# Kernel optimization log

Measured on AMD Instinct MI355X. Metric: run time of the kernel, lower is better.

Reference implementation:

```python
import jax, jax.numpy as jnp
import numpy as np

D_SIZE = 64
BATCH = 4096

def setup_inputs() -> dict:
    key = jax.random.key(0)
    n_vec = D_SIZE * (D_SIZE - 1) // 2  # 2016
    S_vec = jax.random.normal(key, (BATCH, n_vec), dtype=jnp.float32)
    return {"S_vec": S_vec}

def reference(S_vec):
    d = D_SIZE
    iu, ju = np.triu_indices(d, k=1)  # row-major strict upper triangle, same as torch.triu_indices(d, d, 1)
    # Scatter into skew-symmetric matrix: upper = -S_vec, lower = +S_vec
    S = jnp.zeros((*S_vec.shape[:-1], d, d), dtype=S_vec.dtype)
    S = S.at[..., iu, ju].set(-S_vec)
    S = S.at[..., ju, iu].set(S_vec)
    # 1j*S is Hermitian -> real eigenvalues w; original D = w/1j = -1j*w
    w, V = jnp.linalg.eigh(1j * S.astype(jnp.complex64))
    exp_D = jnp.exp(-1j * w)  # exp(D) with D purely imaginary
    # (V * exp_D) @ V^H, take real part (exp of skew-sym is real orthogonal)
    out = (V * exp_D[..., None, :]) @ jnp.conj(jnp.swapaxes(V, -1, -2))
    return out.real
```

## Files before the change

kernel.cpp:

```cpp
#include <hip/hip_runtime.h>
#include <math.h>

#define NVEC 2016
#define NT   256
#define KMAX 8

typedef __attribute__((ext_vector_type(8))) short short8;
typedef __attribute__((ext_vector_type(4))) float v4f;

#define MFMA(a,b,c) __builtin_amdgcn_mfma_f32_16x16x32_bf16((a),(b),(c),0,0,0)

static __device__ __forceinline__ unsigned cvtpk(float a, float b){
    unsigned r;
    asm("v_cvt_pk_bf16_f32 %0, %1, %2" : "=v"(r) : "v"(a), "v"(b));
    return r;
}

static __device__ __forceinline__ void pack_hl4(const float x[4], uint2 &H, uint2 &L){
    H.x = cvtpk(x[0], x[1]);
    H.y = cvtpk(x[2], x[3]);
    float r0 = x[0] - __uint_as_float(H.x << 16);
    float r1 = x[1] - __uint_as_float(H.x & 0xFFFF0000u);
    float r2 = x[2] - __uint_as_float(H.y << 16);
    float r3 = x[3] - __uint_as_float(H.y & 0xFFFF0000u);
    L.x = cvtpk(r0, r1);
    L.y = cvtpk(r2, r3);
}

static __device__ __forceinline__ int swz(int maj, int g){ return maj*64 + ((g ^ (maj & 7)) << 3); }
static __device__ __forceinline__ int swe(int maj, int t){ return swz(maj, t >> 3) + (t & 7); }

static __device__ __forceinline__ short8 ldp(const unsigned short* P, int maj, int off){
    return *(const short8*)&P[swz(maj, off >> 3)];
}

static __device__ __forceinline__ short8 neg8(short8 a){
    union { unsigned u[4]; short8 s; } X; X.s = a;
    X.u[0]^=0x80008000u; X.u[1]^=0x80008000u; X.u[2]^=0x80008000u; X.u[3]^=0x80008000u;
    return X.s;
}

static __device__ __forceinline__ void pair4(const unsigned short* Ph, const unsigned short* Pl,
                                             int cc, int row0, float o[4]){
    const int base = swe(cc, row0);
    uint2 h = *(const uint2*)&Ph[base];
    uint2 l = *(const uint2*)&Pl[base];
    o[0] = __uint_as_float(h.x<<16)           + __uint_as_float(l.x<<16);
    o[1] = __uint_as_float(h.x & 0xFFFF0000u) + __uint_as_float(l.x & 0xFFFF0000u);
    o[2] = __uint_as_float(h.y<<16)           + __uint_as_float(l.y<<16);
    o[3] = __uint_as_float(h.y & 0xFFFF0000u) + __uint_as_float(l.y & 0xFFFF0000u);
}

static __device__ __forceinline__ void pair4h(const unsigned short* Ph, int cc, int row0, float o[4]){
    const uint2 h = *(const uint2*)&Ph[swe(cc, row0)];
    o[0] = __uint_as_float(h.x<<16);
    o[1] = __uint_as_float(h.x & 0xFFFF0000u);
    o[2] = __uint_as_float(h.y<<16);
    o[3] = __uint_as_float(h.y & 0xFFFF0000u);
}

__global__ void __launch_bounds__(NT, 4)
SkewSymMatrixExp_kernel(const float* __restrict__ vin, float* __restrict__ out)
{
    __shared__ __attribute__((aligned(16))) unsigned short PAh[4096];
    __shared__ __attribute__((aligned(16))) unsigned short PAl[4096];
    __shared__ __attribute__((aligned(16))) unsigned short P2h[4096];
    __shared__ __attribute__((aligned(16))) unsigned short P2l[4096];
    __shared__ __attribute__((aligned(16))) unsigned short P4h[4096];

    const int tid  = threadIdx.x;
    const int wave = tid >> 6;
    const int lane = tid & 63;
    const int q    = lane >> 4;
    const int m    = lane & 15;
    const int Rw   = (wave >> 1) * 32;
    const int Cw   = (wave & 1) * 32;
    const float* v = vin + (size_t)blockIdx.x * NVEC;

    {
        const uint4 z4 = make_uint4(0u,0u,0u,0u);
        for (int i = tid; i < 512; i += NT){ ((uint4*)PAh)[i] = z4; ((uint4*)PAl)[i] = z4; }
    }
    __syncthreads();

    for (int p = tid; p < NVEC; p += NT) {
        int i = (int)((127.0f - sqrtf(16129.0f - 8.0f * (float)p)) * 0.5f);
        if (i < 0) i = 0;
        if (i > 62) i = 62;
        while (i > 0 && (63*i - ((i*(i-1))>>1)) > p) --i;
        while (i < 62 && (63*(i+1) - (((i+1)*i)>>1)) <= p) ++i;
        const int off = 63*i - ((i*(i-1))>>1);
        const int j = i + 1 + (p - off);
        const float x = v[p];
        const unsigned hp = cvtpk(x, x) & 0xFFFFu;
        const float    r  = x - __uint_as_float(hp << 16);
        const unsigned lp = cvtpk(r, r) & 0xFFFFu;
        PAh[swe(j, i)] = (unsigned short)(hp ^ 0x8000u);
        PAl[swe(j, i)] = (unsigned short)(lp ^ 0x8000u);
        PAh[swe(i, j)] = (unsigned short)hp;
        PAl[swe(i, j)] = (unsigned short)lp;
    }
    __syncthreads();

    short8 Ah[2][2], Al[2][2];
#pragma unroll
    for (int i=0;i<2;++i)
#pragma unroll
        for (int c=0;c<2;++c){
            Ah[i][c] = neg8(ldp(PAh, Rw+16*i+m, 32*c+8*q));
            Al[i][c] = neg8(ldp(PAl, Rw+16*i+m, 32*c+8*q));
        }

    v4f acc[2][2];

#pragma unroll
    for (int i=0;i<2;++i)
#pragma unroll
        for (int j=0;j<2;++j) acc[i][j] = (v4f){0.f,0.f,0.f,0.f};
#pragma unroll
    for (int c=0;c<2;++c)
#pragma unroll
        for (int j=0;j<2;++j){
            short8 bh = ldp(PAh, Cw+16*j+m, 32*c+8*q);
            short8 bl = ldp(PAl, Cw+16*j+m, 32*c+8*q);
#pragma unroll
            for (int i=0;i<2;++i){
                acc[i][j] = MFMA(Ah[i][c], bh, acc[i][j]);
                acc[i][j] = MFMA(Al[i][c], bh, acc[i][j]);
                acc[i][j] = MFMA(Ah[i][c], bl, acc[i][j]);
            }
        }
#pragma unroll
    for (int i=0;i<2;++i)
#pragma unroll
        for (int j=0;j<2;++j){
            const int row0 = Rw+16*i+4*q, cc = Cw+16*j+m;
            const float x4[4] = { acc[i][j][0], acc[i][j][1], acc[i][j][2], acc[i][j][3] };
            uint2 H, L; pack_hl4(x4, H, L);
            const int base = swe(cc, row0);
            *(uint2*)&P2h[base] = H;
            *(uint2*)&P2l[base] = L;
        }
    __syncthreads();

    float* scratch = (float*)P4h;
    {
        const int c0 = tid & 63, seg = tid >> 6;
        float s = 0.f;
#pragma unroll
        for (int gg=0; gg<2; ++gg){
            const uint4 w = *(const uint4*)&P2h[swz(c0, 2*seg+gg)];
            const unsigned ws[4] = {w.x, w.y, w.z, w.w};
#pragma unroll
            for (int e=0;e<4;++e){
                s += __uint_as_float((ws[e] & 0x7FFFu) << 16);
                s += __uint_as_float(ws[e] & 0x7FFF0000u);
            }
        }
        scratch[tid] = s;
    }
    __syncthreads();
    int kq; float s1, s2, s4;
    {
        float s = scratch[lane] + scratch[lane+64] + scratch[lane+128] + scratch[lane+192];
#pragma unroll
        for (int o=1;o<64;o<<=1) s = fmaxf(s, __shfl_xor(s, o, 64));
        float est = sqrtf(s) * 0.625f;
        kq = 0;
        if (est > 1.f) kq = (int)ceilf(log2f(est));
        if (kq > KMAX) kq = KMAX;
        s1 = exp2f(-(float)kq);
        s2 = s1*s1; s4 = s2*s2;
    }
    __syncthreads();

#pragma unroll
    for (int i=0;i<2;++i)
#pragma unroll
        for (int j=0;j<2;++j) acc[i][j] = (v4f){0.f,0.f,0.f,0.f};
#pragma unroll
    for (int c=0;c<2;++c){
        short8 a2h[2], a2l[2];
#pragma unroll
        for (int i=0;i<2;++i){
            a2h[i] = ldp(P2h, Rw+16*i+m, 32*c+8*q);
            a2l[i] = ldp(P2l, Rw+16*i+m, 32*c+8*q);
        }
#pragma unroll
        for (int j=0;j<2;++j){
            short8 bh = ldp(P2h, Cw+16*j+m, 32*c+8*q);
            short8 bl = ldp(P2l, Cw+16*j+m, 32*c+8*q);
#pragma unroll
            for (int i=0;i<2;++i){
                acc[i][j] = MFMA(a2h[i], bh, acc[i][j]);
                acc[i][j] = MFMA(a2l[i], bh, acc[i][j]);
                acc[i][j] = MFMA(a2h[i], bl, acc[i][j]);
            }
        }
    }
#pragma unroll
    for (int i=0;i<2;++i)
#pragma unroll
        for (int j=0;j<2;++j){
            const int row0 = Rw+16*i+4*q, cc = Cw+16*j+m;
            uint2 H;
            H.x = cvtpk(s4*acc[i][j][0], s4*acc[i][j][1]);
            H.y = cvtpk(s4*acc[i][j][2], s4*acc[i][j][3]);
            *(uint2*)&P4h[swe(cc,row0)] = H;
        }
    __syncthreads();

    v4f accA[2][2], accB[2][2];
#pragma unroll
    for (int i=0;i<2;++i)
#pragma unroll
        for (int j=0;j<2;++j){ accA[i][j] = (v4f){0.f,0.f,0.f,0.f}; accB[i][j] = (v4f){0.f,0.f,0.f,0.f}; }
#pragma unroll
    for (int c=0;c<2;++c){
        short8 a4f[2];
#pragma unroll
        for (int i=0;i<2;++i) a4f[i] = ldp(P4h, Rw+16*i+m, 32*c+8*q);
#pragma unroll
        for (int j=0;j<2;++j){
            short8 b2 = ldp(P2h, Cw+16*j+m, 32*c+8*q);
            short8 b4 = ldp(P4h, Cw+16*j+m, 32*c+8*q);
#pragma unroll
            for (int i=0;i<2;++i){
                accA[i][j] = MFMA(a4f[i], b2, accA[i][j]);
                accB[i][j] = MFMA(a4f[i], b4, accB[i][j]);
            }
        }
    }

    {
        const float ca3 = s2*(1.f/5040.f), cb3 = 1.f/362880.f;
#pragma unroll
        for (int i=0;i<2;++i)
#pragma unroll
            for (int j=0;j<2;++j){
                const int row0 = Rw+16*i+4*q, cc = Cw+16*j+m;
                float e2[4], e4[4];
                pair4(P2h, P2l, cc, row0, e2);
                pair4h(P4h, cc, row0, e4);
                float x4[4];
#pragma unroll
                for (int r=0;r<4;++r)
                    x4[r] = s1*( ca3*accA[i][j][r] + cb3*accB[i][j][r]
                                 + e2[r]*(s2/6.f) + e4[r]*(1.f/120.f)
                                 + ((row0+r)==cc ? 1.f : 0.f) );
                uint2 H, L; pack_hl4(x4, H, L);
                const int base = swe(cc, row0);
                *(uint2*)&PAh[base] = H;
                *(uint2*)&PAl[base] = L;
            }
    }
    __syncthreads();

    {
        const float ca4 = s2*(1.f/720.f), cb4 = 1.f/40320.f;
#pragma unroll
        for (int i=0;i<2;++i)
#pragma unroll
            for (int j=0;j<2;++j)
#pragma unroll
                for (int r=0;r<4;++r)
                    acc[i][j][r] = ca4*accA[i][j][r] + cb4*accB[i][j][r];
    }
#pragma unroll
    for (int c=0;c<2;++c)
#pragma unroll
        for (int j=0;j<2;++j){
            short8 vfh = ldp(PAh, Cw+16*j+m, 32*c+8*q);
            short8 vfl = ldp(PAl, Cw+16*j+m, 32*c+8*q);
#pragma unroll
            for (int i=0;i<2;++i){
                acc[i][j] = MFMA(Ah[i][c], vfh, acc[i][j]);
                acc[i][j] = MFMA(Al[i][c], vfh, acc[i][j]);
                acc[i][j] = MFMA(Ah[i][c], vfl, acc[i][j]);
            }
        }
    {
        float e2[2][2][4], e4[2][2][4];
#pragma unroll
        for (int i=0;i<2;++i)
#pragma unroll
            for (int j=0;j<2;++j){
                pair4(P2h, P2l, Cw+16*j+m, Rw+16*i+4*q, e2[i][j]);
                pair4h(P4h, Cw+16*j+m, Rw+16*i+4*q, e4[i][j]);
            }
        __syncthreads();

#pragma unroll
        for (int i=0;i<2;++i)
#pragma unroll
            for (int j=0;j<2;++j){
                const int row0 = Rw+16*i+4*q, cc = Cw+16*j+m;
                float x4[4];
#pragma unroll
                for (int r=0;r<4;++r)
                    x4[r] = acc[i][j][r] + e2[i][j][r]*(s2*0.5f) + e4[i][j][r]*(1.f/24.f)
                          + ((row0+r)==cc ? 1.f : 0.f);
                if (kq == 0){
                    float* po = out + (size_t)blockIdx.x * 4096;
#pragma unroll
                    for (int r=0;r<4;++r) po[(unsigned)(row0+r)*64 + cc] = x4[r];
                } else {
                    uint2 H, L; pack_hl4(x4, H, L);
                    const int base = swe(cc, row0);
                    *(uint2*)&PAh[base] = H;
                    *(uint2*)&PAl[base] = L;
                    P2h[swe(row0+0, cc)] = (unsigned short)(H.x);
                    P2h[swe(row0+1, cc)] = (unsigned short)(H.x >> 16);
                    P2h[swe(row0+2, cc)] = (unsigned short)(H.y);
                    P2h[swe(row0+3, cc)] = (unsigned short)(H.y >> 16);
                    P2l[swe(row0+0, cc)] = (unsigned short)(L.x);
                    P2l[swe(row0+1, cc)] = (unsigned short)(L.x >> 16);
                    P2l[swe(row0+2, cc)] = (unsigned short)(L.y);
                    P2l[swe(row0+3, cc)] = (unsigned short)(L.y >> 16);
                }
            }
    }
    __syncthreads();

#pragma unroll 1
    for (int s = 0; s < kq; ++s){
#pragma unroll
        for (int i=0;i<2;++i)
#pragma unroll
            for (int j=0;j<2;++j) acc[i][j] = (v4f){0.f,0.f,0.f,0.f};
#pragma unroll
        for (int c=0;c<2;++c){
            short8 xh[2], xl[2];
#pragma unroll
            for (int i=0;i<2;++i){
                xh[i] = ldp(P2h, Rw+16*i+m, 32*c+8*q);
                xl[i] = ldp(P2l, Rw+16*i+m, 32*c+8*q);
            }
#pragma unroll
            for (int j=0;j<2;++j){
                short8 bh = ldp(PAh, Cw+16*j+m, 32*c+8*q);
                short8 bl = ldp(PAl, Cw+16*j+m, 32*c+8*q);
#pragma unroll
                for (int i=0;i<2;++i){
                    acc[i][j] = MFMA(xh[i], bh, acc[i][j]);
                    acc[i][j] = MFMA(xl[i], bh, acc[i][j]);
                    acc[i][j] = MFMA(xh[i], bl, acc[i][j]);
                }
            }
        }
        __syncthreads();

        if (s == kq-1){
            float* po = out + (size_t)blockIdx.x * 4096;
#pragma unroll
            for (int i=0;i<2;++i)
#pragma unroll
                for (int j=0;j<2;++j){
                    const int row0 = Rw+16*i+4*q, cc = Cw+16*j+m;
#pragma unroll
                    for (int r=0;r<4;++r) po[(unsigned)(row0+r)*64 + cc] = acc[i][j][r];
                }
        } else {
#pragma unroll
            for (int i=0;i<2;++i)
#pragma unroll
                for (int j=0;j<2;++j){
                    const int row0 = Rw+16*i+4*q, cc = Cw+16*j+m;
                    const float x4[4] = { acc[i][j][0], acc[i][j][1], acc[i][j][2], acc[i][j][3] };
                    uint2 H, L; pack_hl4(x4, H, L);
                    const int base = swe(cc, row0);
                    *(uint2*)&PAh[base] = H;
                    *(uint2*)&PAl[base] = L;
                    P2h[swe(row0+0, cc)] = (unsigned short)(H.x);
                    P2h[swe(row0+1, cc)] = (unsigned short)(H.x >> 16);
                    P2h[swe(row0+2, cc)] = (unsigned short)(H.y);
                    P2h[swe(row0+3, cc)] = (unsigned short)(H.y >> 16);
                    P2l[swe(row0+0, cc)] = (unsigned short)(L.x);
                    P2l[swe(row0+1, cc)] = (unsigned short)(L.x >> 16);
                    P2l[swe(row0+2, cc)] = (unsigned short)(L.y);
                    P2l[swe(row0+3, cc)] = (unsigned short)(L.y >> 16);
                }
            __syncthreads();
        }
    }
}

extern "C" void kernel_launch(void* const* d_in, const int* in_sizes, int n_in,
                              void* d_out, int out_size, void* d_ws, size_t ws_size,
                              hipStream_t stream) {
    const float* vin = (const float*)d_in[0];
    float* out = (float*)d_out;
    const int batch = in_sizes[0] / NVEC;
    hipLaunchKernelGGL(SkewSymMatrixExp_kernel, dim3(batch), dim3(NT), 0, stream,
                       vin, out);
}
```

Before: 151.6 us.

## Use 8 waves per block with 16x32 per-wave tiles and precomputed LDS offsets

```diff
diff --git a/kernel.cpp b/kernel.cpp
--- a/kernel.cpp
+++ b/kernel.cpp
@@ -2,7 +2,7 @@
 #include <math.h>
 
 #define NVEC 2016
-#define NT   256
+#define NT   512
 #define KMAX 8
 
 typedef __attribute__((ext_vector_type(8))) short short8;
@@ -30,8 +30,8 @@
 static __device__ __forceinline__ int swz(int maj, int g){ return maj*64 + ((g ^ (maj & 7)) << 3); }
 static __device__ __forceinline__ int swe(int maj, int t){ return swz(maj, t >> 3) + (t & 7); }
 
-static __device__ __forceinline__ short8 ldp(const unsigned short* P, int maj, int off){
-    return *(const short8*)&P[swz(maj, off >> 3)];
+static __device__ __forceinline__ short8 ld8(const unsigned short* P, int idx){
+    return *(const short8*)&P[idx];
 }
 
 static __device__ __forceinline__ short8 neg8(short8 a){
@@ -40,9 +40,8 @@
     return X.s;
 }
 
-static __device__ __forceinline__ void pair4(const unsigned short* Ph, const unsigned short* Pl,
-                                             int cc, int row0, float o[4]){
-    const int base = swe(cc, row0);
+static __device__ __forceinline__ void pair4i(const unsigned short* Ph, const unsigned short* Pl,
+                                              int base, float o[4]){
     uint2 h = *(const uint2*)&Ph[base];
     uint2 l = *(const uint2*)&Pl[base];
     o[0] = __uint_as_float(h.x<<16)           + __uint_as_float(l.x<<16);
@@ -51,118 +50,116 @@
     o[3] = __uint_as_float(h.y & 0xFFFF0000u) + __uint_as_float(l.y & 0xFFFF0000u);
 }
 
-static __device__ __forceinline__ void pair4h(const unsigned short* Ph, int cc, int row0, float o[4]){
-    const uint2 h = *(const uint2*)&Ph[swe(cc, row0)];
+static __device__ __forceinline__ void pair4hi(const unsigned short* Ph, int base, float o[4]){
+    const uint2 h = *(const uint2*)&Ph[base];
     o[0] = __uint_as_float(h.x<<16);
     o[1] = __uint_as_float(h.x & 0xFFFF0000u);
     o[2] = __uint_as_float(h.y<<16);
     o[3] = __uint_as_float(h.y & 0xFFFF0000u);
 }
 
-__global__ void __launch_bounds__(NT, 4)
+__global__ void __launch_bounds__(NT, 8)
 SkewSymMatrixExp_kernel(const float* __restrict__ vin, float* __restrict__ out)
 {
-    __shared__ __attribute__((aligned(16))) unsigned short PAh[4096];
-    __shared__ __attribute__((aligned(16))) unsigned short PAl[4096];
-    __shared__ __attribute__((aligned(16))) unsigned short P2h[4096];
-    __shared__ __attribute__((aligned(16))) unsigned short P2l[4096];
-    __shared__ __attribute__((aligned(16))) unsigned short P4h[4096];
+    __shared__ __attribute__((aligned(16))) unsigned short LDS[5*4096];
+    unsigned short* const PAh = LDS;
+    unsigned short* const PAl = LDS + 4096;
+    unsigned short* const P2h = LDS + 8192;
+    unsigned short* const P2l = LDS + 12288;
+    unsigned short* const P4h = LDS + 16384;
 
     const int tid  = threadIdx.x;
     const int wave = tid >> 6;
     const int lane = tid & 63;
     const int q    = lane >> 4;
     const int m    = lane & 15;
-    const int Rw   = (wave >> 1) * 32;
-    const int Cw   = (wave & 1) * 32;
+    const int Rw16 = (wave >> 1) * 16;
+    const int Cw32 = (wave & 1) * 32;
+    const int row0 = Rw16 + 4*q;
     const float* v = vin + (size_t)blockIdx.x * NVEC;
 
-    {
-        const uint4 z4 = make_uint4(0u,0u,0u,0u);
-        for (int i = tid; i < 512; i += NT){ ((uint4*)PAh)[i] = z4; ((uint4*)PAl)[i] = z4; }
-    }
-    __syncthreads();
-
+    const int rdA[2] = { swz(Rw16+m, q), swz(Rw16+m, 4+q) };
+    int rdB[2][2], wrF[2];
+#pragma unroll
+    for (int j=0;j<2;++j){
+        const int cc = Cw32 + 16*j + m;
+        rdB[j][0] = swz(cc, q);
+        rdB[j][1] = swz(cc, 4+q);
+        wrF[j]    = swe(cc, row0);
+    }
+
+    if (tid < 64){
+        const int d = swe(tid, tid);
+        PAh[d] = 0; PAl[d] = 0;
+    }
     for (int p = tid; p < NVEC; p += NT) {
-        int i = (int)((127.0f - sqrtf(16129.0f - 8.0f * (float)p)) * 0.5f);
-        if (i < 0) i = 0;
-        if (i > 62) i = 62;
-        while (i > 0 && (63*i - ((i*(i-1))>>1)) > p) --i;
-        while (i < 62 && (63*(i+1) - (((i+1)*i)>>1)) <= p) ++i;
-        const int off = 63*i - ((i*(i-1))>>1);
-        const int j = i + 1 + (p - off);
+        int ii = (int)((127.0f - sqrtf(16129.0f - 8.0f * (float)p)) * 0.5f);
+        if (ii < 0) ii = 0;
+        if (ii > 62) ii = 62;
+        while (ii > 0 && (63*ii - ((ii*(ii-1))>>1)) > p) --ii;
+        while (ii < 62 && (63*(ii+1) - (((ii+1)*ii)>>1)) <= p) ++ii;
+        const int off = 63*ii - ((ii*(ii-1))>>1);
+        const int jj = ii + 1 + (p - off);
         const float x = v[p];
         const unsigned hp = cvtpk(x, x) & 0xFFFFu;
-        const float    r  = x - __uint_as_float(hp << 16);
-        const unsigned lp = cvtpk(r, r) & 0xFFFFu;
-        PAh[swe(j, i)] = (unsigned short)(hp ^ 0x8000u);
-        PAl[swe(j, i)] = (unsigned short)(lp ^ 0x8000u);
-        PAh[swe(i, j)] = (unsigned short)hp;
-        PAl[swe(i, j)] = (unsigned short)lp;
-    }
-    __syncthreads();
-
-    short8 Ah[2][2], Al[2][2];
-#pragma unroll
-    for (int i=0;i<2;++i)
-#pragma unroll
-        for (int c=0;c<2;++c){
-            Ah[i][c] = neg8(ldp(PAh, Rw+16*i+m, 32*c+8*q));
-            Al[i][c] = neg8(ldp(PAl, Rw+16*i+m, 32*c+8*q));
-        }
-
-    v4f acc[2][2];
-
-#pragma unroll
-    for (int i=0;i<2;++i)
-#pragma unroll
-        for (int j=0;j<2;++j) acc[i][j] = (v4f){0.f,0.f,0.f,0.f};
+        const float    rr = x - __uint_as_float(hp << 16);
+        const unsigned lp = cvtpk(rr, rr) & 0xFFFFu;
+        PAh[swe(jj, ii)] = (unsigned short)(hp ^ 0x8000u);
+        PAl[swe(jj, ii)] = (unsigned short)(lp ^ 0x8000u);
+        PAh[swe(ii, jj)] = (unsigned short)hp;
+        PAl[swe(ii, jj)] = (unsigned short)lp;
+    }
+    __syncthreads();
+
+    short8 Ah[2], Al[2];
+#pragma unroll
+    for (int c=0;c<2;++c){
+        Ah[c] = neg8(ld8(PAh, rdA[c]));
+        Al[c] = neg8(ld8(PAl, rdA[c]));
+    }
+
+    v4f acc[2];
+
+#pragma unroll
+    for (int j=0;j<2;++j) acc[j] = (v4f){0.f,0.f,0.f,0.f};
 #pragma unroll
     for (int c=0;c<2;++c)
 #pragma unroll
         for (int j=0;j<2;++j){
-            short8 bh = ldp(PAh, Cw+16*j+m, 32*c+8*q);
-            short8 bl = ldp(PAl, Cw+16*j+m, 32*c+8*q);
-#pragma unroll
-            for (int i=0;i<2;++i){
-                acc[i][j] = MFMA(Ah[i][c], bh, acc[i][j]);
-                acc[i][j] = MFMA(Al[i][c], bh, acc[i][j]);
-                acc[i][j] = MFMA(Ah[i][c], bl, acc[i][j]);
-            }
-        }
-#pragma unroll
-    for (int i=0;i<2;++i)
-#pragma unroll
-        for (int j=0;j<2;++j){
-            const int row0 = Rw+16*i+4*q, cc = Cw+16*j+m;
-            const float x4[4] = { acc[i][j][0], acc[i][j][1], acc[i][j][2], acc[i][j][3] };
-            uint2 H, L; pack_hl4(x4, H, L);
-            const int base = swe(cc, row0);
-            *(uint2*)&P2h[base] = H;
-            *(uint2*)&P2l[base] = L;
-        }
+            short8 bh = ld8(PAh, rdB[j][c]);
+            short8 bl = ld8(PAl, rdB[j][c]);
+            acc[j] = MFMA(Ah[c], bh, acc[j]);
+            acc[j] = MFMA(Al[c], bh, acc[j]);
+            acc[j] = MFMA(Ah[c], bl, acc[j]);
+        }
+#pragma unroll
+    for (int j=0;j<2;++j){
+        const float x4[4] = { acc[j][0], acc[j][1], acc[j][2], acc[j][3] };
+        uint2 H, L; pack_hl4(x4, H, L);
+        *(uint2*)&P2h[wrF[j]] = H;
+        *(uint2*)&P2l[wrF[j]] = L;
+    }
     __syncthreads();
 
     float* scratch = (float*)P4h;
     {
         const int c0 = tid & 63, seg = tid >> 6;
+        const uint4 w = *(const uint4*)&P2h[swz(c0, seg)];
+        const unsigned ws[4] = {w.x, w.y, w.z, w.w};
         float s = 0.f;
 #pragma unroll
-        for (int gg=0; gg<2; ++gg){
-            const uint4 w = *(const uint4*)&P2h[swz(c0, 2*seg+gg)];
-            const unsigned ws[4] = {w.x, w.y, w.z, w.w};
-#pragma unroll
-            for (int e=0;e<4;++e){
-                s += __uint_as_float((ws[e] & 0x7FFFu) << 16);
-                s += __uint_as_float(ws[e] & 0x7FFF0000u);
-            }
+        for (int e=0;e<4;++e){
+            s += __uint_as_float((ws[e] & 0x7FFFu) << 16);
+            s += __uint_as_float(ws[e] & 0x7FFF0000u);
         }
         scratch[tid] = s;
     }
     __syncthreads();
     int kq; float s1, s2, s4;
     {
-        float s = scratch[lane] + scratch[lane+64] + scratch[lane+128] + scratch[lane+192];
+        float s = 0.f;
+#pragma unroll
+        for (int k=0;k<8;++k) s += scratch[lane + 64*k];
 #pragma unroll
         for (int o=1;o<64;o<<=1) s = fmaxf(s, __shfl_xor(s, o, 64));
         float est = sqrtf(s) * 0.625f;
@@ -175,211 +172,167 @@
     __syncthreads();
 
 #pragma unroll
-    for (int i=0;i<2;++i)
-#pragma unroll
-        for (int j=0;j<2;++j) acc[i][j] = (v4f){0.f,0.f,0.f,0.f};
+    for (int j=0;j<2;++j) acc[j] = (v4f){0.f,0.f,0.f,0.f};
 #pragma unroll
     for (int c=0;c<2;++c){
-        short8 a2h[2], a2l[2];
-#pragma unroll
-        for (int i=0;i<2;++i){
-            a2h[i] = ldp(P2h, Rw+16*i+m, 32*c+8*q);
-            a2l[i] = ldp(P2l, Rw+16*i+m, 32*c+8*q);
-        }
-#pragma unroll
-        for (int j=0;j<2;++j){
-            short8 bh = ldp(P2h, Cw+16*j+m, 32*c+8*q);
-            short8 bl = ldp(P2l, Cw+16*j+m, 32*c+8*q);
-#pragma unroll
-            for (int i=0;i<2;++i){
-                acc[i][j] = MFMA(a2h[i], bh, acc[i][j]);
-                acc[i][j] = MFMA(a2l[i], bh, acc[i][j]);
-                acc[i][j] = MFMA(a2h[i], bl, acc[i][j]);
-            }
-        }
-    }
-#pragma unroll
-    for (int i=0;i<2;++i)
-#pragma unroll
-        for (int j=0;j<2;++j){
-            const int row0 = Rw+16*i+4*q, cc = Cw+16*j+m;
-            uint2 H;
-            H.x = cvtpk(s4*acc[i][j][0], s4*acc[i][j][1]);
-            H.y = cvtpk(s4*acc[i][j][2], s4*acc[i][j][3]);
-            *(uint2*)&P4h[swe(cc,row0)] = H;
-        }
-    __syncthreads();
-
-    v4f accA[2][2], accB[2][2];
-#pragma unroll
-    for (int i=0;i<2;++i)
-#pragma unroll
-        for (int j=0;j<2;++j){ accA[i][j] = (v4f){0.f,0.f,0.f,0.f}; accB[i][j] = (v4f){0.f,0.f,0.f,0.f}; }
+        short8 a2h = ld8(P2h, rdA[c]);
+        short8 a2l = ld8(P2l, rdA[c]);
+#pragma unroll
+        for (int j=0;j<2;++j){
+            short8 bh = ld8(P2h, rdB[j][c]);
+            short8 bl = ld8(P2l, rdB[j][c]);
+            acc[j] = MFMA(a2h, bh, acc[j]);
+            acc[j] = MFMA(a2l, bh, acc[j]);
+            acc[j] = MFMA(a2h, bl, acc[j]);
+        }
+    }
+#pragma unroll
+    for (int j=0;j<2;++j){
+        uint2 H;
+        H.x = cvtpk(s4*acc[j][0], s4*acc[j][1]);
+        H.y = cvtpk(s4*acc[j][2], s4*acc[j][3]);
+        *(uint2*)&P4h[wrF[j]] = H;
+    }
+    __syncthreads();
+
+    v4f accA[2], accB[2];
+#pragma unroll
+    for (int j=0;j<2;++j){ accA[j] = (v4f){0.f,0.f,0.f,0.f}; accB[j] = (v4f){0.f,0.f,0.f,0.f}; }
 #pragma unroll
     for (int c=0;c<2;++c){
-        short8 a4f[2];
-#pragma unroll
-        for (int i=0;i<2;++i) a4f[i] = ldp(P4h, Rw+16*i+m, 32*c+8*q);
-#pragma unroll
-        for (int j=0;j<2;++j){
-            short8 b2 = ldp(P2h, Cw+16*j+m, 32*c+8*q);
-            short8 b4 = ldp(P4h, Cw+16*j+m, 32*c+8*q);
-#pragma unroll
-            for (int i=0;i<2;++i){
-                accA[i][j] = MFMA(a4f[i], b2, accA[i][j]);
-                accB[i][j] = MFMA(a4f[i], b4, accB[i][j]);
-            }
+        short8 a4 = ld8(P4h, rdA[c]);
+#pragma unroll
+        for (int j=0;j<2;++j){
+            short8 b2 = ld8(P2h, rdB[j][c]);
+            short8 b4 = ld8(P4h, rdB[j][c]);
+            accA[j] = MFMA(a4, b2, accA[j]);
+            accB[j] = MFMA(a4, b4, accB[j]);
         }
     }
 
     {
         const float ca3 = s2*(1.f/5040.f), cb3 = 1.f/362880.f;
 #pragma unroll
-        for (int i=0;i<2;++i)
-#pragma unroll
-            for (int j=0;j<2;++j){
-                const int row0 = Rw+16*i+4*q, cc = Cw+16*j+m;
-                float e2[4], e4[4];
-                pair4(P2h, P2l, cc, row0, e2);
-                pair4h(P4h, cc, row0, e4);
-                float x4[4];
-#pragma unroll
-                for (int r=0;r<4;++r)
-                    x4[r] = s1*( ca3*accA[i][j][r] + cb3*accB[i][j][r]
-                                 + e2[r]*(s2/6.f) + e4[r]*(1.f/120.f)
-                                 + ((row0+r)==cc ? 1.f : 0.f) );
+        for (int j=0;j<2;++j){
+            const int cc = Cw32 + 16*j + m;
+            float e2[4], e4[4];
+            pair4i(P2h, P2l, wrF[j], e2);
+            pair4hi(P4h, wrF[j], e4);
+            float x4[4];
+#pragma unroll
+            for (int r=0;r<4;++r)
+                x4[r] = s1*( ca3*accA[j][r] + cb3*accB[j][r]
+                             + e2[r]*(s2/6.f) + e4[r]*(1.f/120.f)
+                             + ((row0+r)==cc ? 1.f : 0.f) );
+            uint2 H, L; pack_hl4(x4, H, L);
+            *(uint2*)&PAh[wrF[j]] = H;
+            *(uint2*)&PAl[wrF[j]] = L;
+        }
+    }
+    __syncthreads();
+
+    {
+        const float ca4 = s2*(1.f/720.f), cb4 = 1.f/40320.f;
+#pragma unroll
+        for (int j=0;j<2;++j)
+#pragma unroll
+            for (int r=0;r<4;++r)
+                acc[j][r] = ca4*accA[j][r] + cb4*accB[j][r];
+    }
+#pragma unroll
+    for (int c=0;c<2;++c)
+#pragma unroll
+        for (int j=0;j<2;++j){
+            short8 vfh = ld8(PAh, rdB[j][c]);
+            short8 vfl = ld8(PAl, rdB[j][c]);
+            acc[j] = MFMA(Ah[c], vfh, acc[j]);
+            acc[j] = MFMA(Al[c], vfh, acc[j]);
+            acc[j] = MFMA(Ah[c], vfl, acc[j]);
+        }
+    {
+        float e2[2][4], e4[2][4];
+#pragma unroll
+        for (int j=0;j<2;++j){
+            pair4i(P2h, P2l, wrF[j], e2[j]);
+            pair4hi(P4h, wrF[j], e4[j]);
+        }
+        __syncthreads();
+
+#pragma unroll
+        for (int j=0;j<2;++j){
+            const int cc = Cw32 + 16*j + m;
+            float x4[4];
+#pragma unroll
+            for (int r=0;r<4;++r)
+                x4[r] = acc[j][r] + e2[j][r]*(s2*0.5f) + e4[j][r]*(1.f/24.f)
+                      + ((row0+r)==cc ? 1.f : 0.f);
+            if (kq == 0){
+                float* po = out + (size_t)blockIdx.x * 4096;
+#pragma unroll
+                for (int r=0;r<4;++r) po[(unsigned)(row0+r)*64 + cc] = x4[r];
+            } else {
                 uint2 H, L; pack_hl4(x4, H, L);
-                const int base = swe(cc, row0);
-                *(uint2*)&PAh[base] = H;
-                *(uint2*)&PAl[base] = L;
-            }
-    }
-    __syncthreads();
-
-    {
-        const float ca4 = s2*(1.f/720.f), cb4 = 1.f/40320.f;
-#pragma unroll
-        for (int i=0;i<2;++i)
-#pragma unroll
-            for (int j=0;j<2;++j)
-#pragma unroll
-                for (int r=0;r<4;++r)
-                    acc[i][j][r] = ca4*accA[i][j][r] + cb4*accB[i][j][r];
-    }
-#pragma unroll
-    for (int c=0;c<2;++c)
-#pragma unroll
-        for (int j=0;j<2;++j){
-            short8 vfh = ldp(PAh, Cw+16*j+m, 32*c+8*q);
-            short8 vfl = ldp(PAl, Cw+16*j+m, 32*c+8*q);
-#pragma unroll
-            for (int i=0;i<2;++i){
-                acc[i][j] = MFMA(Ah[i][c], vfh, acc[i][j]);
-                acc[i][j] = MFMA(Al[i][c], vfh, acc[i][j]);
-                acc[i][j] = MFMA(Ah[i][c], vfl, acc[i][j]);
-            }
-        }
-    {
-        float e2[2][2][4], e4[2][2][4];
-#pragma unroll
-        for (int i=0;i<2;++i)
-#pragma unroll
-            for (int j=0;j<2;++j){
-                pair4(P2h, P2l, Cw+16*j+m, Rw+16*i+4*q, e2[i][j]);
-                pair4h(P4h, Cw+16*j+m, Rw+16*i+4*q, e4[i][j]);
-            }
-        __syncthreads();
-
-#pragma unroll
-        for (int i=0;i<2;++i)
-#pragma unroll
-            for (int j=0;j<2;++j){
-                const int row0 = Rw+16*i+4*q, cc = Cw+16*j+m;
-                float x4[4];
-#pragma unroll
-                for (int r=0;r<4;++r)
-                    x4[r] = acc[i][j][r] + e2[i][j][r]*(s2*0.5f) + e4[i][j][r]*(1.f/24.f)
-                          + ((row0+r)==cc ? 1.f : 0.f);
-                if (kq == 0){
-                    float* po = out + (size_t)blockIdx.x * 4096;
-#pragma unroll
-                    for (int r=0;r<4;++r) po[(unsigned)(row0+r)*64 + cc] = x4[r];
-                } else {
-                    uint2 H, L; pack_hl4(x4, H, L);
-                    const int base = swe(cc, row0);
-                    *(uint2*)&PAh[base] = H;
-                    *(uint2*)&PAl[base] = L;
-                    P2h[swe(row0+0, cc)] = (unsigned short)(H.x);
-                    P2h[swe(row0+1, cc)] = (unsigned short)(H.x >> 16);
-                    P2h[swe(row0+2, cc)] = (unsigned short)(H.y);
-                    P2h[swe(row0+3, cc)] = (unsigned short)(H.y >> 16);
-                    P2l[swe(row0+0, cc)] = (unsigned short)(L.x);
-                    P2l[swe(row0+1, cc)] = (unsigned short)(L.x >> 16);
-                    P2l[swe(row0+2, cc)] = (unsigned short)(L.y);
-                    P2l[swe(row0+3, cc)] = (unsigned short)(L.y >> 16);
+                *(uint2*)&PAh[wrF[j]] = H;
+                *(uint2*)&PAl[wrF[j]] = L;
+                const int gj = cc >> 3, c7 = cc & 7, rb = row0 & 7;
+                const unsigned hr[4] = { H.x & 0xFFFFu, H.x >> 16, H.y & 0xFFFFu, H.y >> 16 };
+                const unsigned lr[4] = { L.x & 0xFFFFu, L.x >> 16, L.y & 0xFFFFu, L.y >> 16 };
+#pragma unroll
+                for (int r=0;r<4;++r){
+                    const int idx = (row0+r)*64 + ((gj ^ (rb+r)) << 3) + c7;
+                    P2h[idx] = (unsigned short)hr[r];
+                    P2l[idx] = (unsigned short)lr[r];
                 }
             }
+        }
     }
     __syncthreads();
 
 #pragma unroll 1
     for (int s = 0; s < kq; ++s){
 #pragma unroll
-        for (int i=0;i<2;++i)
-#pragma unroll
-            for (int j=0;j<2;++j) acc[i][j] = (v4f){0.f,0.f,0.f,0.f};
+        for (int j=0;j<2;++j) acc[j] = (v4f){0.f,0.f,0.f,0.f};
 #pragma unroll
         for (int c=0;c<2;++c){
-            short8 xh[2], xl[2];
-#pragma unroll
-            for (int i=0;i<2;++i){
-                xh[i] = ldp(P2h, Rw+16*i+m, 32*c+8*q);
-                xl[i] = ldp(P2l, Rw+16*i+m, 32*c+8*q);
+            short8 xh = ld8(P2h, rdA[c]);
+            short8 xl = ld8(P2l, rdA[c]);
+#pragma unroll
+            for (int j=0;j<2;++j){
+                short8 bh = ld8(PAh, rdB[j][c]);
+                short8 bl = ld8(PAl, rdB[j][c]);
+                acc[j] = MFMA(xh, bh, acc[j]);
+                acc[j] = MFMA(xl, bh, acc[j]);
+                acc[j] = MFMA(xh, bl, acc[j]);
             }
+        }
+        __syncthreads();
+
+        if (s == kq-1){
+            float* po = out + (size_t)blockIdx.x * 4096;
 #pragma unroll
             for (int j=0;j<2;++j){
-                short8 bh = ldp(PAh, Cw+16*j+m, 32*c+8*q);
-                short8 bl = ldp(PAl, Cw+16*j+m, 32*c+8*q);
-#pragma unroll
-                for (int i=0;i<2;++i){
-                    acc[i][j] = MFMA(xh[i], bh, acc[i][j]);
-                    acc[i][j] = MFMA(xl[i], bh, acc[i][j]);
-                    acc[i][j] = MFMA(xh[i], bl, acc[i][j]);
+                const int cc = Cw32 + 16*j + m;
+#pragma unroll
+                for (int r=0;r<4;++r) po[(unsigned)(row0+r)*64 + cc] = acc[j][r];
+            }
+        } else {
+#pragma unroll
+            for (int j=0;j<2;++j){
+                const int cc = Cw32 + 16*j + m;
+                const float x4[4] = { acc[j][0], acc[j][1], acc[j][2], acc[j][3] };
+                uint2 H, L; pack_hl4(x4, H, L);
+                *(uint2*)&PAh[wrF[j]] = H;
+                *(uint2*)&PAl[wrF[j]] = L;
+                const int gj = cc >> 3, c7 = cc & 7, rb = row0 & 7;
+                const unsigned hr[4] = { H.x & 0xFFFFu, H.x >> 16, H.y & 0xFFFFu, H.y >> 16 };
+                const unsigned lr[4] = { L.x & 0xFFFFu, L.x >> 16, L.y & 0xFFFFu, L.y >> 16 };
+#pragma unroll
+                for (int r=0;r<4;++r){
+                    const int idx = (row0+r)*64 + ((gj ^ (rb+r)) << 3) + c7;
+                    P2h[idx] = (unsigned short)hr[r];
+                    P2l[idx] = (unsigned short)lr[r];
                 }
             }
-        }
-        __syncthreads();
-
-        if (s == kq-1){
-            float* po = out + (size_t)blockIdx.x * 4096;
-#pragma unroll
-            for (int i=0;i<2;++i)
-#pragma unroll
-                for (int j=0;j<2;++j){
-                    const int row0 = Rw+16*i+4*q, cc = Cw+16*j+m;
-#pragma unroll
-                    for (int r=0;r<4;++r) po[(unsigned)(row0+r)*64 + cc] = acc[i][j][r];
-                }
-        } else {
-#pragma unroll
-            for (int i=0;i<2;++i)
-#pragma unroll
-                for (int j=0;j<2;++j){
-                    const int row0 = Rw+16*i+4*q, cc = Cw+16*j+m;
-                    const float x4[4] = { acc[i][j][0], acc[i][j][1], acc[i][j][2], acc[i][j][3] };
-                    uint2 H, L; pack_hl4(x4, H, L);
-                    const int base = swe(cc, row0);
-                    *(uint2*)&PAh[base] = H;
-                    *(uint2*)&PAl[base] = L;
-                    P2h[swe(row0+0, cc)] = (unsigned short)(H.x);
-                    P2h[swe(row0+1, cc)] = (unsigned short)(H.x >> 16);
-                    P2h[swe(row0+2, cc)] = (unsigned short)(H.y);
-                    P2h[swe(row0+3, cc)] = (unsigned short)(H.y >> 16);
-                    P2l[swe(row0+0, cc)] = (unsigned short)(L.x);
-                    P2l[swe(row0+1, cc)] = (unsigned short)(L.x >> 16);
-                    P2l[swe(row0+2, cc)] = (unsigned short)(L.y);
-                    P2l[swe(row0+3, cc)] = (unsigned short)(L.y >> 16);
-                }
             __syncthreads();
         }
     }
```

Measured after the change: 153.9 us. No clear change (+1.5%).
